# Optimization experiments

Hardware: AMD Instinct MI355X
Metric: run time of the kernel (lower is better)

The kernel has to match this reference:

```python
import jax, jax.numpy as jnp
import numpy as np

N_NODES = 50000
N_EDGES = 1600000


def gcn_conv(h, W, b, src, dst, ew, n_nodes):
    """PyG GCNConv: linear -> add self-loops (weight 1) -> sym-norm scatter-add -> bias."""
    h = h @ W                                   # [N, out]
    loop = jnp.arange(n_nodes, dtype=src.dtype)
    s = jnp.concatenate([src, loop])            # [E+N]
    d = jnp.concatenate([dst, loop])
    w = jnp.concatenate([ew, jnp.ones((n_nodes,), dtype=h.dtype)])
    deg = jax.ops.segment_sum(w, d, num_segments=n_nodes)          # in-degree (weighted)
    dinv = jnp.where(deg > 0, jax.lax.rsqrt(deg), 0.0)
    coef = dinv[s] * w * dinv[d]                # D^-1/2 A D^-1/2 per-edge coefficient
    msg = h[s] * coef[:, None]                  # gather + scale  [E+N, out]
    out = jax.ops.segment_sum(msg, d, num_segments=n_nodes)        # scatter-add
    return out + b


def setup_inputs() -> dict:
    key = jax.random.key(0)
    ks = jax.random.split(key, 6)
    x = jax.random.normal(ks[0], (N_NODES, 256), dtype=jnp.float32)
    edge_index = jax.random.randint(ks[1], (2, N_EDGES), 0, N_NODES, dtype=jnp.int64)
    edge_weight = jax.random.uniform(ks[2], (N_EDGES,), dtype=jnp.float32)
    W1 = jax.random.normal(ks[3], (256, 128), dtype=jnp.float32) * (1.0 / np.sqrt(256))
    b1 = jnp.zeros((128,), dtype=jnp.float32)
    W2 = jax.random.normal(ks[4], (128, 64), dtype=jnp.float32) * (1.0 / np.sqrt(128))
    b2 = jnp.zeros((64,), dtype=jnp.float32)
    return {"x": x, "edge_index": edge_index, "edge_weight": edge_weight,
            "W1": W1, "b1": b1, "W2": W2, "b2": b2}


def reference(x, edge_index, edge_weight, W1, b1, W2, b2):
    src, dst = edge_index[0], edge_index[1]
    n = x.shape[0]
    h = gcn_conv(x, W1, b1, src, dst, edge_weight, n)
    h = jax.nn.relu(h)
    # dropout is identity in eval mode
    out = gcn_conv(h, W2, b2, src, dst, edge_weight, n)
    return out
```

## Files before the change

kernel.cpp:

```cpp
#include <hip/hip_runtime.h>

#define NN 50000
#define NE 1600000
#define NB 391
#define NBLK 128
#define NSEG 50048

typedef short bf16x8 __attribute__((ext_vector_type(8)));
typedef float f32x4 __attribute__((ext_vector_type(4)));

static __device__ __forceinline__ unsigned f2bf(float f) {
    union { float f; unsigned u; } v; v.f = f;
    return (v.u + 0x7FFF + ((v.u >> 16) & 1)) >> 16;
}

__global__ __launch_bounds__(256) void p1_hist(const int* __restrict__ dst,
        int* __restrict__ cntB) {
    __shared__ int h[NB];
    for (int i = threadIdx.x; i < NB; i += 256) h[i] = 0;
    __syncthreads();
    int base = blockIdx.x * 12500;
    for (int k = threadIdx.x; k < 12500; k += 256)
        atomicAdd(&h[dst[base + k] >> 7], 1);
    __syncthreads();
    for (int i = threadIdx.x; i < NB; i += 256)
        cntB[i * NBLK + blockIdx.x] = h[i];
}

__global__ __launch_bounds__(256) void scan1_kernel(const int* __restrict__ in,
        int* __restrict__ csum, int* __restrict__ bsum) {
    __shared__ int sd[256];
    int t = threadIdx.x;
    int idx = blockIdx.x * 256 + t;
    int v = (idx < NSEG) ? in[idx] : 0;
    sd[t] = v;
    __syncthreads();
    for (int off = 1; off < 256; off <<= 1) {
        int x = (t >= off) ? sd[t - off] : 0;
        __syncthreads();
        sd[t] += x;
        __syncthreads();
    }
    if (idx < NSEG) csum[idx + 1] = sd[t];
    if (t == 255) bsum[blockIdx.x] = sd[255];
}

__global__ __launch_bounds__(256) void scan2_kernel(int* __restrict__ bsum,
        int* __restrict__ csum) {
    __shared__ int sd[256];
    int t = threadIdx.x;
    int v = (t < 196) ? bsum[t] : 0;
    sd[t] = v;
    __syncthreads();
    for (int off = 1; off < 256; off <<= 1) {
        int x = (t >= off) ? sd[t - off] : 0;
        __syncthreads();
        sd[t] += x;
        __syncthreads();
    }
    if (t < 196) bsum[t] = sd[t] - v;
    if (t == 0) csum[0] = 0;
}

__global__ __launch_bounds__(256) void scan3_kernel(int* __restrict__ csum,
        const int* __restrict__ bsum) {
    int idx = blockIdx.x * 256 + threadIdx.x;
    if (idx < NSEG) csum[idx + 1] += bsum[blockIdx.x];
}

__global__ __launch_bounds__(256) void p3_scatter(const int* __restrict__ src,
        const int* __restrict__ dst, const float* __restrict__ ew,
        const int* __restrict__ csum, int2* __restrict__ ebuf) {
    __shared__ int curs[NB];
    for (int i = threadIdx.x; i < NB; i += 256)
        curs[i] = csum[i * NBLK + blockIdx.x];
    __syncthreads();
    int base = blockIdx.x * 12500;
    for (int k = threadIdx.x; k < 12500; k += 256) {
        int d = dst[base + k];
        int s = src[base + k];
        float w = ew[base + k];
        int pos = atomicAdd(&curs[d >> 7], 1);
        ebuf[pos] = make_int2(s | ((d & 127) << 16), __float_as_int(w));
    }
}

__global__ __launch_bounds__(256) void p4_build(const int2* __restrict__ ebuf,
        const int* __restrict__ csum, int2* __restrict__ edata,
        float* __restrict__ dinv, int* __restrict__ rowptr) {
    __shared__ int cnt[128], loff[128], cur[128], sd[128];
    __shared__ float deg[128];
    int bk = blockIdx.x;
    int t = threadIdx.x;
    int ebase = csum[bk * 128];
    int eend  = csum[(bk + 1) * 128];
    int ecnt = eend - ebase;
    if (t < 128) { cnt[t] = 0; cur[t] = 0; deg[t] = 0.0f; }
    __syncthreads();
    for (int i = t; i < ecnt; i += 256) {
        int2 e = ebuf[ebase + i];
        int dl = (e.x >> 16) & 127;
        atomicAdd(&cnt[dl], 1);
        atomicAdd(&deg[dl], __int_as_float(e.y));
    }
    __syncthreads();
    if (t < 128) sd[t] = cnt[t];
    __syncthreads();
    for (int off = 1; off < 128; off <<= 1) {
        int v = 0;
        if (t < 128 && t >= off) v = sd[t - off];
        __syncthreads();
        if (t < 128) sd[t] += v;
        __syncthreads();
    }
    if (t < 128) loff[t] = sd[t] - cnt[t];
    __syncthreads();
    int node = bk * 128 + t;
    if (t < 128 && node < NN) {
        dinv[node] = rsqrtf(deg[t] + 1.0f);
        rowptr[node] = ebase + loff[t];
    }
    if (bk == NB - 1 && t == 0) rowptr[NN] = NE;
    for (int i = t; i < ecnt; i += 256) {
        int2 e = ebuf[ebase + i];
        int dl = (e.x >> 16) & 127;
        int slot = loff[dl] + atomicAdd(&cur[dl], 1);
        edata[ebase + slot] = make_int2(e.x & 0xFFFF, e.y);
    }
}

__global__ __launch_bounds__(256) void coef_kernel(int2* __restrict__ edata,
        const float* __restrict__ dinv) {
    int i = blockIdx.x * 256 + threadIdx.x;
    if (i >= NE) return;
    int2 e = edata[i];
    edata[i].y = __float_as_int(dinv[e.x] * __int_as_float(e.y));
}

__global__ __launch_bounds__(256) void wt_kernel(const float* __restrict__ W,
        ushort* __restrict__ Wt, int K, int nshift) {
    int idx = blockIdx.x * 256 + threadIdx.x;
    if (idx >= (K << nshift)) return;
    int k = idx >> nshift, n = idx & ((1 << nshift) - 1);
    Wt[(size_t)n * K + k] = (ushort)f2bf(W[idx]);
}

__global__ __launch_bounds__(256) void gemm_a32_kernel(const float* __restrict__ A,
        const ushort* __restrict__ Bt, ushort* __restrict__ C, int M, int N, int K) {
    __shared__ __align__(16) ushort As[64][72];
    __shared__ __align__(16) ushort Bs[64][72];
    int tid = threadIdx.x;
    int bm = blockIdx.y * 64, bn = blockIdx.x * 64;
    int w = tid >> 6, lane = tid & 63;
    int m = lane & 15, quad = lane >> 4;
    f32x4 acc[4] = {};
    int r = tid >> 2, ks0 = (tid & 3) * 16;
    int grow = bm + r; if (grow >= M) grow = M - 1;
    const float* ap = A + (size_t)grow * K + ks0;
    const ushort* bp = Bt + (size_t)(bn + r) * K + ks0;
    for (int k0 = 0; k0 < K; k0 += 64) {
        float4 f0 = *(const float4*)(ap + k0);
        float4 f1 = *(const float4*)(ap + k0 + 4);
        float4 f2 = *(const float4*)(ap + k0 + 8);
        float4 f3 = *(const float4*)(ap + k0 + 12);
        uint4 bv0 = *(const uint4*)(bp + k0);
        uint4 bv1 = *(const uint4*)(bp + k0 + 8);
        uint4 pa, pb;
        pa.x = f2bf(f0.x) | (f2bf(f0.y) << 16);
        pa.y = f2bf(f0.z) | (f2bf(f0.w) << 16);
        pa.z = f2bf(f1.x) | (f2bf(f1.y) << 16);
        pa.w = f2bf(f1.z) | (f2bf(f1.w) << 16);
        pb.x = f2bf(f2.x) | (f2bf(f2.y) << 16);
        pb.y = f2bf(f2.z) | (f2bf(f2.w) << 16);
        pb.z = f2bf(f3.x) | (f2bf(f3.y) << 16);
        pb.w = f2bf(f3.z) | (f2bf(f3.w) << 16);
        __syncthreads();
        *(uint4*)&As[r][ks0] = pa;
        *(uint4*)&As[r][ks0 + 8] = pb;
        *(uint4*)&Bs[r][ks0] = bv0;
        *(uint4*)&Bs[r][ks0 + 8] = bv1;
        __syncthreads();
        #pragma unroll
        for (int ks = 0; ks < 2; ++ks) {
            bf16x8 a = *(const bf16x8*)&As[w * 16 + m][ks * 32 + quad * 8];
            #pragma unroll
            for (int t = 0; t < 4; ++t) {
                bf16x8 b = *(const bf16x8*)&Bs[t * 16 + m][ks * 32 + quad * 8];
                acc[t] = __builtin_amdgcn_mfma_f32_16x16x32_bf16(a, b, acc[t], 0, 0, 0);
            }
        }
    }
    #pragma unroll
    for (int t = 0; t < 4; ++t) {
        int col = bn + t * 16 + m;
        #pragma unroll
        for (int rg = 0; rg < 4; ++rg) {
            int row = bm + w * 16 + quad * 4 + rg;
            if (row < M) C[(size_t)row * N + col] = (ushort)f2bf(acc[t][rg]);
        }
    }
}

__global__ __launch_bounds__(256) void gemm_a16_kernel(const ushort* __restrict__ A,
        const ushort* __restrict__ Bt, ushort* __restrict__ C, int M, int N, int K) {
    __shared__ __align__(16) ushort As[64][72];
    __shared__ __align__(16) ushort Bs[64][72];
    int tid = threadIdx.x;
    int bm = blockIdx.y * 64, bn = blockIdx.x * 64;
    int w = tid >> 6, lane = tid & 63;
    int m = lane & 15, quad = lane >> 4;
    f32x4 acc[4] = {};
    int r = tid >> 2, ks0 = (tid & 3) * 16;
    int grow = bm + r; if (grow >= M) grow = M - 1;
    const ushort* ap = A + (size_t)grow * K + ks0;
    const ushort* bp = Bt + (size_t)(bn + r) * K + ks0;
    for (int k0 = 0; k0 < K; k0 += 64) {
        uint4 av0 = *(const uint4*)(ap + k0);
        uint4 av1 = *(const uint4*)(ap + k0 + 8);
        uint4 bv0 = *(const uint4*)(bp + k0);
        uint4 bv1 = *(const uint4*)(bp + k0 + 8);
        __syncthreads();
        *(uint4*)&As[r][ks0] = av0;
        *(uint4*)&As[r][ks0 + 8] = av1;
        *(uint4*)&Bs[r][ks0] = bv0;
        *(uint4*)&Bs[r][ks0 + 8] = bv1;
        __syncthreads();
        #pragma unroll
        for (int ks = 0; ks < 2; ++ks) {
            bf16x8 a = *(const bf16x8*)&As[w * 16 + m][ks * 32 + quad * 8];
            #pragma unroll
            for (int t = 0; t < 4; ++t) {
                bf16x8 b = *(const bf16x8*)&Bs[t * 16 + m][ks * 32 + quad * 8];
                acc[t] = __builtin_amdgcn_mfma_f32_16x16x32_bf16(a, b, acc[t], 0, 0, 0);
            }
        }
    }
    #pragma unroll
    for (int t = 0; t < 4; ++t) {
        int col = bn + t * 16 + m;
        #pragma unroll
        for (int rg = 0; rg < 4; ++rg) {
            int row = bm + w * 16 + quad * 4 + rg;
            if (row < M) C[(size_t)row * N + col] = (ushort)f2bf(acc[t][rg]);
        }
    }
}

template<int F, int LPN, int RELU, int OUTBF>
__global__ __launch_bounds__(256) void agg_csr_kernel(
        const int* __restrict__ rowptr, const int2* __restrict__ edata,
        const ushort* __restrict__ H, const float* __restrict__ dinv,
        const float* __restrict__ bias, void* __restrict__ outv) {
    constexpr int NPB = 256 / LPN;
    int node = blockIdx.x * NPB + threadIdx.x / LPN;
    if (node >= NN) return;
    int glane = threadIdx.x & (LPN - 1);
    int gb = (threadIdx.x & 63) & ~(LPN - 1);
    int beg = rowptr[node], end = rowptr[node + 1];
    float acc[8] = {};
    const ushort* Hl = H + (size_t)glane * 8;
    for (int chunk = beg; chunk < end; chunk += LPN) {
        int nch = end - chunk; if (nch > LPN) nch = LPN;
        int2 ed = make_int2(0, 0);
        if (glane < nch) ed = edata[chunk + glane];
        int j = 0;
        for (; j + 2 <= nch; j += 2) {
            int s0 = __shfl(ed.x, gb + j);
            float c0 = __int_as_float(__shfl(ed.y, gb + j));
            int s1 = __shfl(ed.x, gb + j + 1);
            float c1 = __int_as_float(__shfl(ed.y, gb + j + 1));
            uint4 h0 = *(const uint4*)(Hl + (size_t)s0 * F);
            uint4 h1 = *(const uint4*)(Hl + (size_t)s1 * F);
            const unsigned* u0 = (const unsigned*)&h0;
            const unsigned* u1 = (const unsigned*)&h1;
            #pragma unroll
            for (int q = 0; q < 4; ++q) {
                acc[2*q]   += __uint_as_float(u0[q] << 16) * c0;
                acc[2*q+1] += __uint_as_float(u0[q] & 0xFFFF0000u) * c0;
            }
            #pragma unroll
            for (int q = 0; q < 4; ++q) {
                acc[2*q]   += __uint_as_float(u1[q] << 16) * c1;
                acc[2*q+1] += __uint_as_float(u1[q] & 0xFFFF0000u) * c1;
            }
        }
        if (j < nch) {
            int s0 = __shfl(ed.x, gb + j);
            float c0 = __int_as_float(__shfl(ed.y, gb + j));
            uint4 h0 = *(const uint4*)(Hl + (size_t)s0 * F);
            const unsigned* u0 = (const unsigned*)&h0;
            #pragma unroll
            for (int q = 0; q < 4; ++q) {
                acc[2*q]   += __uint_as_float(u0[q] << 16) * c0;
                acc[2*q+1] += __uint_as_float(u0[q] & 0xFFFF0000u) * c0;
            }
        }
    }
    float di = dinv[node];
    float sc = di * di;
    uint4 hn = *(const uint4*)(Hl + (size_t)node * F);
    const unsigned* un = (const unsigned*)&hn;
    float4 bv0 = *(const float4*)(bias + glane * 8);
    float4 bv1 = *(const float4*)(bias + glane * 8 + 4);
    float v[8];
    #pragma unroll
    for (int q = 0; q < 4; ++q) {
        v[2*q]   = di * acc[2*q]   + sc * __uint_as_float(un[q] << 16);
        v[2*q+1] = di * acc[2*q+1] + sc * __uint_as_float(un[q] & 0xFFFF0000u);
    }
    v[0] += bv0.x; v[1] += bv0.y; v[2] += bv0.z; v[3] += bv0.w;
    v[4] += bv1.x; v[5] += bv1.y; v[6] += bv1.z; v[7] += bv1.w;
    if (RELU) {
        #pragma unroll
        for (int k = 0; k < 8; ++k) v[k] = fmaxf(v[k], 0.0f);
    }
    if (OUTBF) {
        uint4 o;
        o.x = f2bf(v[0]) | (f2bf(v[1]) << 16);
        o.y = f2bf(v[2]) | (f2bf(v[3]) << 16);
        o.z = f2bf(v[4]) | (f2bf(v[5]) << 16);
        o.w = f2bf(v[6]) | (f2bf(v[7]) << 16);
        *(uint4*)((ushort*)outv + (size_t)node * F + glane * 8) = o;
    } else {
        float* o = (float*)outv + (size_t)node * F + glane * 8;
        *(float4*)(o)     = make_float4(v[0], v[1], v[2], v[3]);
        *(float4*)(o + 4) = make_float4(v[4], v[5], v[6], v[7]);
    }
}

extern "C" void kernel_launch(void* const* d_in, const int* in_sizes, int n_in,
                              void* d_out, int out_size, void* d_ws, size_t ws_size,
                              hipStream_t stream) {
    const float* x  = (const float*)d_in[0];
    const int*   ei = (const int*)d_in[1];
    const float* ew = (const float*)d_in[2];
    const float* W1 = (const float*)d_in[3];
    const float* b1 = (const float*)d_in[4];
    const float* W2 = (const float*)d_in[5];
    const float* b2 = (const float*)d_in[6];
    const int* src = ei;
    const int* dst = ei + NE;
    float* out = (float*)d_out;

    float* ws     = (float*)d_ws;
    float* dinv   = ws;
    int*   rowptr = (int*)(ws + 50048);
    int*   csum   = (int*)(ws + 100112);
    int*   bsum   = (int*)(ws + 150176);
    int*   cntB   = (int*)(ws + 150528);
    ushort* Wt1   = (ushort*)(ws + 200576);
    ushort* Wt2   = Wt1 + 32768;
    int2*  edata  = (int2*)(ws + 221056);
    ushort* H1    = (ushort*)(ws + 3421056);
    ushort* A1    = (ushort*)(ws + 6621056);
    int2*  ebuf   = (int2*)A1;

    p1_hist<<<NBLK, 256, 0, stream>>>(dst, cntB);
    scan1_kernel<<<196, 256, 0, stream>>>(cntB, csum, bsum);
    scan2_kernel<<<1, 256, 0, stream>>>(bsum, csum);
    scan3_kernel<<<196, 256, 0, stream>>>(csum, bsum);
    wt_kernel<<<128, 256, 0, stream>>>(W1, Wt1, 256, 7);
    wt_kernel<<<32, 256, 0, stream>>>(W2, Wt2, 128, 6);
    p3_scatter<<<NBLK, 256, 0, stream>>>(src, dst, ew, csum, ebuf);
    p4_build<<<NB, 256, 0, stream>>>(ebuf, csum, edata, dinv, rowptr);
    coef_kernel<<<NE / 256, 256, 0, stream>>>(edata, dinv);

    gemm_a32_kernel<<<dim3(2, 782), 256, 0, stream>>>(x, Wt1, H1, NN, 128, 256);
    agg_csr_kernel<128, 16, 1, 1><<<3125, 256, 0, stream>>>(rowptr, edata, H1, dinv, b1, A1);

    gemm_a16_kernel<<<dim3(1, 782), 256, 0, stream>>>(A1, Wt2, H1, NN, 64, 128);
    agg_csr_kernel<64, 8, 0, 0><<<1563, 256, 0, stream>>>(rowptr, edata, H1, dinv, b2, out);
}
```

Before: 278.8 us.

## Fold source dinv into GEMM epilogue, drop coef pass, cache edges in LDS

The per-edge coefficient kernel is removed: the source-side dinv scale now happens in the GEMM epilogues (H scaled by dinv per row), and the aggregation applies dinv of the destination to the sum including the self term. p4_build stages edge records in shared memory when they fit, avoiding a second global read. Nontemporal loads are used for streaming edge inputs, the two weight-transpose launches are merged, and the aggregation gather loop is unrolled to four edges. Rounding H after scaling slightly changes the bf16 rounding, and the 36KB LDS buffer may reduce p4_build occupancy.

```diff
diff --git a/kernel.cpp b/kernel.cpp
--- a/kernel.cpp
+++ b/kernel.cpp
@@ -20,8 +20,10 @@
     for (int i = threadIdx.x; i < NB; i += 256) h[i] = 0;
     __syncthreads();
     int base = blockIdx.x * 12500;
-    for (int k = threadIdx.x; k < 12500; k += 256)
-        atomicAdd(&h[dst[base + k] >> 7], 1);
+    for (int k = threadIdx.x; k < 12500; k += 256) {
+        int d = __builtin_nontemporal_load(dst + base + k);
+        atomicAdd(&h[d >> 7], 1);
+    }
     __syncthreads();
     for (int i = threadIdx.x; i < NB; i += 256)
         cntB[i * NBLK + blockIdx.x] = h[i];
@@ -77,9 +79,9 @@
     __syncthreads();
     int base = blockIdx.x * 12500;
     for (int k = threadIdx.x; k < 12500; k += 256) {
-        int d = dst[base + k];
-        int s = src[base + k];
-        float w = ew[base + k];
+        int d = __builtin_nontemporal_load(dst + base + k);
+        int s = __builtin_nontemporal_load(src + base + k);
+        float w = __builtin_nontemporal_load(ew + base + k);
         int pos = atomicAdd(&curs[d >> 7], 1);
         ebuf[pos] = make_int2(s | ((d & 127) << 16), __float_as_int(w));
     }
@@ -90,15 +92,18 @@
         float* __restrict__ dinv, int* __restrict__ rowptr) {
     __shared__ int cnt[128], loff[128], cur[128], sd[128];
     __shared__ float deg[128];
+    __shared__ int2 se[4608];
     int bk = blockIdx.x;
     int t = threadIdx.x;
     int ebase = csum[bk * 128];
-    int eend  = csum[(bk + 1) * 128];
-    int ecnt = eend - ebase;
+    int ecnt = csum[(bk + 1) * 128] - ebase;
+    bool fit = (ecnt <= 4608);
     if (t < 128) { cnt[t] = 0; cur[t] = 0; deg[t] = 0.0f; }
     __syncthreads();
     for (int i = t; i < ecnt; i += 256) {
-        int2 e = ebuf[ebase + i];
+        long long raw = __builtin_nontemporal_load((const long long*)(ebuf + ebase + i));
+        int2 e = make_int2((int)raw, (int)(raw >> 32));
+        if (fit) se[i] = e;
         int dl = (e.x >> 16) & 127;
         atomicAdd(&cnt[dl], 1);
         atomicAdd(&deg[dl], __int_as_float(e.y));
@@ -122,31 +127,30 @@
     }
     if (bk == NB - 1 && t == 0) rowptr[NN] = NE;
     for (int i = t; i < ecnt; i += 256) {
-        int2 e = ebuf[ebase + i];
+        int2 e = fit ? se[i] : ebuf[ebase + i];
         int dl = (e.x >> 16) & 127;
         int slot = loff[dl] + atomicAdd(&cur[dl], 1);
         edata[ebase + slot] = make_int2(e.x & 0xFFFF, e.y);
     }
 }
 
-__global__ __launch_bounds__(256) void coef_kernel(int2* __restrict__ edata,
-        const float* __restrict__ dinv) {
-    int i = blockIdx.x * 256 + threadIdx.x;
-    if (i >= NE) return;
-    int2 e = edata[i];
-    edata[i].y = __float_as_int(dinv[e.x] * __int_as_float(e.y));
-}
-
-__global__ __launch_bounds__(256) void wt_kernel(const float* __restrict__ W,
-        ushort* __restrict__ Wt, int K, int nshift) {
+__global__ __launch_bounds__(256) void wt_kernel(const float* __restrict__ W1,
+        const float* __restrict__ W2, ushort* __restrict__ Wt1,
+        ushort* __restrict__ Wt2) {
     int idx = blockIdx.x * 256 + threadIdx.x;
-    if (idx >= (K << nshift)) return;
-    int k = idx >> nshift, n = idx & ((1 << nshift) - 1);
-    Wt[(size_t)n * K + k] = (ushort)f2bf(W[idx]);
+    if (idx < 32768) {
+        int k = idx >> 7, n = idx & 127;
+        Wt1[n * 256 + k] = (ushort)f2bf(W1[idx]);
+    } else if (idx < 40960) {
+        int i = idx - 32768;
+        int k = i >> 6, n = i & 63;
+        Wt2[n * 128 + k] = (ushort)f2bf(W2[i]);
+    }
 }
 
 __global__ __launch_bounds__(256) void gemm_a32_kernel(const float* __restrict__ A,
-        const ushort* __restrict__ Bt, ushort* __restrict__ C, int M, int N, int K) {
+        const ushort* __restrict__ Bt, ushort* __restrict__ C,
+        const float* __restrict__ dinv, int M, int N, int K) {
     __shared__ __align__(16) ushort As[64][72];
     __shared__ __align__(16) ushort Bs[64][72];
     int tid = threadIdx.x;
@@ -190,19 +194,25 @@
             }
         }
     }
+    int rbase = bm + w * 16 + quad * 4;
+    float dv[4];
+    #pragma unroll
+    for (int rg = 0; rg < 4; ++rg)
+        dv[rg] = (rbase + rg < M) ? dinv[rbase + rg] : 0.0f;
     #pragma unroll
     for (int t = 0; t < 4; ++t) {
         int col = bn + t * 16 + m;
         #pragma unroll
         for (int rg = 0; rg < 4; ++rg) {
-            int row = bm + w * 16 + quad * 4 + rg;
-            if (row < M) C[(size_t)row * N + col] = (ushort)f2bf(acc[t][rg]);
+            int row = rbase + rg;
+            if (row < M) C[(size_t)row * N + col] = (ushort)f2bf(dv[rg] * acc[t][rg]);
         }
     }
 }
 
 __global__ __launch_bounds__(256) void gemm_a16_kernel(const ushort* __restrict__ A,
-        const ushort* __restrict__ Bt, ushort* __restrict__ C, int M, int N, int K) {
+        const ushort* __restrict__ Bt, ushort* __restrict__ C,
+        const float* __restrict__ dinv, int M, int N, int K) {
     __shared__ __align__(16) ushort As[64][72];
     __shared__ __align__(16) ushort Bs[64][72];
     int tid = threadIdx.x;
@@ -235,13 +245,18 @@
             }
         }
     }
+    int rbase = bm + w * 16 + quad * 4;
+    float dv[4];
+    #pragma unroll
+    for (int rg = 0; rg < 4; ++rg)
+        dv[rg] = (rbase + rg < M) ? dinv[rbase + rg] : 0.0f;
     #pragma unroll
     for (int t = 0; t < 4; ++t) {
         int col = bn + t * 16 + m;
         #pragma unroll
         for (int rg = 0; rg < 4; ++rg) {
-            int row = bm + w * 16 + quad * 4 + rg;
-            if (row < M) C[(size_t)row * N + col] = (ushort)f2bf(acc[t][rg]);
+            int row = rbase + rg;
+            if (row < M) C[(size_t)row * N + col] = (ushort)f2bf(dv[rg] * acc[t][rg]);
         }
     }
 }
@@ -261,18 +276,30 @@
     const ushort* Hl = H + (size_t)glane * 8;
     for (int chunk = beg; chunk < end; chunk += LPN) {
         int nch = end - chunk; if (nch > LPN) nch = LPN;
-        int2 ed = make_int2(0, 0);
-        if (glane < nch) ed = edata[chunk + glane];
+        int edx = 0, edy = 0;
+        if (glane < nch) {
+            long long raw = __builtin_nontemporal_load(
+                (const long long*)(edata + chunk + glane));
+            edx = (int)raw; edy = (int)(raw >> 32);
+        }
         int j = 0;
-        for (; j + 2 <= nch; j += 2) {
-            int s0 = __shfl(ed.x, gb + j);
-            float c0 = __int_as_float(__shfl(ed.y, gb + j));
-            int s1 = __shfl(ed.x, gb + j + 1);
-            float c1 = __int_as_float(__shfl(ed.y, gb + j + 1));
+        for (; j + 4 <= nch; j += 4) {
+            int s0 = __shfl(edx, gb + j);
+            int s1 = __shfl(edx, gb + j + 1);
+            int s2 = __shfl(edx, gb + j + 2);
+            int s3 = __shfl(edx, gb + j + 3);
+            float c0 = __int_as_float(__shfl(edy, gb + j));
+            float c1 = __int_as_float(__shfl(edy, gb + j + 1));
+            float c2 = __int_as_float(__shfl(edy, gb + j + 2));
+            float c3 = __int_as_float(__shfl(edy, gb + j + 3));
             uint4 h0 = *(const uint4*)(Hl + (size_t)s0 * F);
             uint4 h1 = *(const uint4*)(Hl + (size_t)s1 * F);
+            uint4 h2 = *(const uint4*)(Hl + (size_t)s2 * F);
+            uint4 h3 = *(const uint4*)(Hl + (size_t)s3 * F);
             const unsigned* u0 = (const unsigned*)&h0;
             const unsigned* u1 = (const unsigned*)&h1;
+            const unsigned* u2 = (const unsigned*)&h2;
+            const unsigned* u3 = (const unsigned*)&h3;
             #pragma unroll
             for (int q = 0; q < 4; ++q) {
                 acc[2*q]   += __uint_as_float(u0[q] << 16) * c0;
@@ -283,10 +310,20 @@
                 acc[2*q]   += __uint_as_float(u1[q] << 16) * c1;
                 acc[2*q+1] += __uint_as_float(u1[q] & 0xFFFF0000u) * c1;
             }
-        }
-        if (j < nch) {
-            int s0 = __shfl(ed.x, gb + j);
-            float c0 = __int_as_float(__shfl(ed.y, gb + j));
+            #pragma unroll
+            for (int q = 0; q < 4; ++q) {
+                acc[2*q]   += __uint_as_float(u2[q] << 16) * c2;
+                acc[2*q+1] += __uint_as_float(u2[q] & 0xFFFF0000u) * c2;
+            }
+            #pragma unroll
+            for (int q = 0; q < 4; ++q) {
+                acc[2*q]   += __uint_as_float(u3[q] << 16) * c3;
+                acc[2*q+1] += __uint_as_float(u3[q] & 0xFFFF0000u) * c3;
+            }
+        }
+        for (; j < nch; ++j) {
+            int s0 = __shfl(edx, gb + j);
+            float c0 = __int_as_float(__shfl(edy, gb + j));
             uint4 h0 = *(const uint4*)(Hl + (size_t)s0 * F);
             const unsigned* u0 = (const unsigned*)&h0;
             #pragma unroll
@@ -297,7 +334,6 @@
         }
     }
     float di = dinv[node];
-    float sc = di * di;
     uint4 hn = *(const uint4*)(Hl + (size_t)node * F);
     const unsigned* un = (const unsigned*)&hn;
     float4 bv0 = *(const float4*)(bias + glane * 8);
@@ -305,8 +341,8 @@
     float v[8];
     #pragma unroll
     for (int q = 0; q < 4; ++q) {
-        v[2*q]   = di * acc[2*q]   + sc * __uint_as_float(un[q] << 16);
-        v[2*q+1] = di * acc[2*q+1] + sc * __uint_as_float(un[q] & 0xFFFF0000u);
+        v[2*q]   = di * (acc[2*q]   + __uint_as_float(un[q] << 16));
+        v[2*q+1] = di * (acc[2*q+1] + __uint_as_float(un[q] & 0xFFFF0000u));
     }
     v[0] += bv0.x; v[1] += bv0.y; v[2] += bv0.z; v[3] += bv0.w;
     v[4] += bv1.x; v[5] += bv1.y; v[6] += bv1.z; v[7] += bv1.w;
@@ -359,15 +395,13 @@
     scan1_kernel<<<196, 256, 0, stream>>>(cntB, csum, bsum);
     scan2_kernel<<<1, 256, 0, stream>>>(bsum, csum);
     scan3_kernel<<<196, 256, 0, stream>>>(csum, bsum);
-    wt_kernel<<<128, 256, 0, stream>>>(W1, Wt1, 256, 7);
-    wt_kernel<<<32, 256, 0, stream>>>(W2, Wt2, 128, 6);
+    wt_kernel<<<160, 256, 0, stream>>>(W1, W2, Wt1, Wt2);
     p3_scatter<<<NBLK, 256, 0, stream>>>(src, dst, ew, csum, ebuf);
     p4_build<<<NB, 256, 0, stream>>>(ebuf, csum, edata, dinv, rowptr);
-    coef_kernel<<<NE / 256, 256, 0, stream>>>(edata, dinv);
-
-    gemm_a32_kernel<<<dim3(2, 782), 256, 0, stream>>>(x, Wt1, H1, NN, 128, 256);
+
+    gemm_a32_kernel<<<dim3(2, 782), 256, 0, stream>>>(x, Wt1, H1, dinv, NN, 128, 256);
     agg_csr_kernel<128, 16, 1, 1><<<3125, 256, 0, stream>>>(rowptr, edata, H1, dinv, b1, A1);
 
-    gemm_a16_kernel<<<dim3(1, 782), 256, 0, stream>>>(A1, Wt2, H1, NN, 64, 128);
+    gemm_a16_kernel<<<dim3(1, 782), 256, 0, stream>>>(A1, Wt2, H1, dinv, NN, 64, 128);
     agg_csr_kernel<64, 8, 0, 0><<<1563, 256, 0, stream>>>(rowptr, edata, H1, dinv, b2, out);
 }
```

Result: slower. 288.5 us (+3.5%).
